# Optimization experiments

Hardware: AMD Instinct MI355X
Metric: run time of the kernel (lower is better)

The kernel has to match this reference:

```python
import jax, jax.numpy as jnp
import numpy as np
from jax import lax

V, D, L = 32000, 1024, 8
HQ, HKV, HD = 16, 4, 64          # head_dim = D // HQ
H = int(2.6875 * D)              # SwiGLU hidden = 2752
B, S = 2, 1024
WINDOW, GEVERY = 256, 4
EPS, BASE = 1e-6, 10000.0
STD = 0.02


def setup_inputs() -> dict:
    key = jax.random.key(0)
    ks = jax.random.split(key, 10)
    return {
        "idx": jax.random.randint(ks[0], (B, S), 0, V, dtype=jnp.int32),
        "emb": jax.random.normal(ks[1], (V, D), jnp.float32) * STD,
        "Wq": jax.random.normal(ks[2], (L, D, HQ * HD), jnp.float32) * STD,
        "Wk": jax.random.normal(ks[3], (L, D, HKV * HD), jnp.float32) * STD,
        "Wv": jax.random.normal(ks[4], (L, D, HKV * HD), jnp.float32) * STD,
        "Wo": jax.random.normal(ks[5], (L, HQ * HD, D), jnp.float32) * (STD / np.sqrt(2 * L)).astype(np.float32),
        "w1": jax.random.normal(ks[6], (L, D, H), jnp.float32) * STD,
        "w3": jax.random.normal(ks[7], (L, D, H), jnp.float32) * STD,
        "w2": jax.random.normal(ks[8], (L, H, D), jnp.float32) * (STD / np.sqrt(2 * L)).astype(np.float32),
        "n1": jnp.ones((L, D), jnp.float32),
        "n2": jnp.ones((L, D), jnp.float32),
        "nf": jnp.ones((D,), jnp.float32),
    }


def _rmsnorm(x, w):
    return x * lax.rsqrt(jnp.mean(x * x, axis=-1, keepdims=True) + EPS) * w


def _rope(x, cos, sin):
    # x: [B,S,h,HD]; pairs (even, odd) rotated by complex multiply with e^{i*theta}
    x2 = x.reshape(*x.shape[:-1], HD // 2, 2)
    x0, x1 = x2[..., 0], x2[..., 1]
    r0 = x0 * cos - x1 * sin
    r1 = x0 * sin + x1 * cos
    return jnp.stack([r0, r1], axis=-1).reshape(x.shape)


def _forward(idx, emb, Wq, Wk, Wv, Wo, w1, w3, w2, n1, n2, nf):
    # RoPE cache (RoPECache._build_cache)
    inv_freq = 1.0 / (BASE ** (jnp.arange(0, HD, 2, dtype=jnp.float32) / HD))
    t = jnp.arange(S, dtype=jnp.float32)
    freqs = t[:, None] * inv_freq[None, :]                      # [S, HD//2]
    cos = jnp.cos(freqs)[None, :, None, :]                      # [1,S,1,HD//2]
    sin = jnp.sin(freqs)[None, :, None, :]

    # masks: global causal and sliding-window causal (additive, 0 / -inf)
    pos = jnp.arange(S)
    causal = pos[None, :] <= pos[:, None]
    local = causal & ((pos[:, None] - pos[None, :]) < WINDOW)
    neg_inf = jnp.float32(-jnp.inf)
    gmask = jnp.where(causal, 0.0, neg_inf).astype(jnp.float32)
    lmask = jnp.where(local, 0.0, neg_inf).astype(jnp.float32)
    use_global = ((jnp.arange(L) + 1) % GEVERY) == 0            # [L] bool

    scale = 1.0 / (HD ** 0.5)
    rep = HQ // HKV

    def block(x, p):
        wq, wk, wv, wo, W1, W3, W2, g1, g2, ug = p
        h = _rmsnorm(x, g1)
        q = (h @ wq).reshape(B, S, HQ, HD)
        k = (h @ wk).reshape(B, S, HKV, HD)
        v = (h @ wv).reshape(B, S, HKV, HD)
        q = _rope(q, cos, sin)
        k = _rope(k, cos, sin)
        k = jnp.repeat(k, rep, axis=2)                          # GQA: expand KV heads
        v = jnp.repeat(v, rep, axis=2)
        mask = jnp.where(ug, gmask, lmask)
        sc = jnp.einsum('bqhd,bkhd->bhqk', q, k) * scale + mask
        attn = jax.nn.softmax(sc, axis=-1)
        o = jnp.einsum('bhqk,bkhd->bqhd', attn, v).reshape(B, S, HQ * HD)
        x = x + o @ wo
        h2 = _rmsnorm(x, g2)
        x = x + (jax.nn.silu(h2 @ W1) * (h2 @ W3)) @ W2
        return x, None

    x = emb[idx]                                                # token embedding
    x, _ = lax.scan(block, x, (Wq, Wk, Wv, Wo, w1, w3, w2, n1, n2, use_global))
    logits = _rmsnorm(x, nf) @ emb.T                            # tied lm_head
    return logits


def reference(idx, emb, Wq, Wk, Wv, Wo, w1, w3, w2, n1, n2, nf):
    return _forward(idx, emb, Wq, Wk, Wv, Wo, w1, w3, w2, n1, n2, nf)
```

## Files before the change

### kernel.cpp

```cpp
#include <hip/hip_runtime.h>

#define V_ 32000
#define D_ 1024
#define L_ 8
#define HQ_ 16
#define HKV_ 4
#define HD_ 64
#define H_ 2752
#define B_ 2
#define S_ 1024
#define BS_ 2048
#define WINDOW_ 256

typedef float f32x4 __attribute__((ext_vector_type(4)));
typedef short s16x8 __attribute__((ext_vector_type(8)));
typedef unsigned short u16;

__device__ __forceinline__ u16 f2b(float f) {
  union { float f; unsigned u; } a; a.f = f;
  return (u16)((a.u + 0x7fffu + ((a.u >> 16) & 1u)) >> 16);
}
__device__ __forceinline__ float b2f(u16 b) {
  union { unsigned u; float f; } a; a.u = ((unsigned)b) << 16; return a.f;
}

__device__ __forceinline__ void gload_lds16(const void* g, void* l) {
  __builtin_amdgcn_global_load_lds(
      (const __attribute__((address_space(1))) void*)(unsigned long long)(uintptr_t)g,
      (__attribute__((address_space(3))) void*)(unsigned int)(uintptr_t)l,
      16, 0, 0);
}

__global__ void k_init(const float* __restrict__ src, u16* __restrict__ dst,
                       float* __restrict__ cosT, float* __restrict__ sinT,
                       const int* __restrict__ idx, float* __restrict__ x) {
  int bid = blockIdx.x;
  if (bid < 32000) {
    long i = (long)bid * 256 + threadIdx.x;
    float4 v = ((const float4*)src)[i];
    ushort4 o; o.x = f2b(v.x); o.y = f2b(v.y); o.z = f2b(v.z); o.w = f2b(v.w);
    ((ushort4*)dst)[i] = o;
  } else if (bid < 32128) {
    int i = (bid - 32000) * 256 + threadIdx.x;
    int s = i >> 5, d = i & 31;
    float inv = __expf(-((float)(2 * d) / (float)HD_) * logf(10000.0f));
    float f = (float)s * inv;
    cosT[i] = cosf(f); sinT[i] = sinf(f);
  } else {
    int t = bid - 32128;
    int token = idx[t];
    const float4* s = (const float4*)(src + (size_t)token * D_);
    float4* d = (float4*)(x + (size_t)t * D_);
    d[threadIdx.x] = s[threadIdx.x];
  }
}

struct TMat { const float* src; u16* dst; int R, C, t0, mul, add; };
struct T7 { TMat m[7]; };

__global__ void k_transpose7(T7 P) {
  __shared__ float tile[32][33];
  int bid = blockIdx.x;
  int mi = 0;
#pragma unroll
  for (int i = 1; i < 7; ++i) if (bid >= P.m[i].t0) mi = i;
  TMat mm = P.m[mi];
  int tl = bid - mm.t0;
  int ct = mm.C >> 5;
  int tr = tl / ct, tc = tl - tr * ct;
  int r0 = tr << 5, c0 = tc << 5;
  int tx = threadIdx.x & 31, ty = threadIdx.x >> 5;
#pragma unroll
  for (int j = 0; j < 4; ++j)
    tile[ty + j * 8][tx] = mm.src[(size_t)(r0 + ty + j * 8) * mm.C + c0 + tx];
  __syncthreads();
#pragma unroll
  for (int j = 0; j < 4; ++j)
    mm.dst[((size_t)(c0 + ty + j * 8) * mm.mul + mm.add) * mm.R + r0 + tx] =
        f2b(tile[tx][ty + j * 8]);
}

__global__ void k_rmsnorm(const float* __restrict__ x, const float* __restrict__ w,
                          u16* __restrict__ out) {
  int row = blockIdx.x, tid = threadIdx.x;
  float4 v = ((const float4*)(x + (size_t)row * D_))[tid];
  float ss = v.x * v.x + v.y * v.y + v.z * v.z + v.w * v.w;
#pragma unroll
  for (int m = 1; m < 64; m <<= 1) ss += __shfl_xor(ss, m, 64);
  __shared__ float red[4];
  if ((tid & 63) == 0) red[tid >> 6] = ss;
  __syncthreads();
  float tot = red[0] + red[1] + red[2] + red[3];
  float rs = rsqrtf(tot * (1.0f / D_) + 1e-6f);
  float4 wv = ((const float4*)w)[tid];
  ushort4 o;
  o.x = f2b(v.x * rs * wv.x); o.y = f2b(v.y * rs * wv.y);
  o.z = f2b(v.z * rs * wv.z); o.w = f2b(v.w * rs * wv.w);
  ((ushort4*)(out + (size_t)row * D_))[tid] = o;
}

__global__ void k_ropev(const float* __restrict__ qkvf, const float* __restrict__ cosT,
                        const float* __restrict__ sinT, u16* __restrict__ qh,
                        u16* __restrict__ kh, u16* __restrict__ vth) {
  __shared__ float tile[32][65];
  int bid = blockIdx.x;
  int tid = threadIdx.x;
  if (bid < BS_) {
    int t = bid;
    int b = t >> 10, s = t & (S_ - 1);
    const float* row = qkvf + (size_t)t * 1536;
    for (int p = tid; p < 512; p += 256) {
      int hh = p >> 5, d = p & 31;
      float x0 = row[hh * 64 + 2 * d], x1 = row[hh * 64 + 2 * d + 1];
      float c = cosT[s * 32 + d], sn = sinT[s * 32 + d];
      size_t o = ((size_t)(b * HQ_ + hh) * S_ + s) * HD_ + 2 * d;
      qh[o] = f2b(x0 * c - x1 * sn);
      qh[o + 1] = f2b(x0 * sn + x1 * c);
    }
    if (tid < 128) {
      int hh = tid >> 5, d = tid & 31;
      float x0 = row[1024 + hh * 64 + 2 * d], x1 = row[1024 + hh * 64 + 2 * d + 1];
      float c = cosT[s * 32 + d], sn = sinT[s * 32 + d];
      size_t o = ((size_t)(b * HKV_ + hh) * S_ + s) * HD_ + 2 * d;
      kh[o] = f2b(x0 * c - x1 * sn);
      kh[o + 1] = f2b(x0 * sn + x1 * c);
    }
  } else {
    int v = bid - BS_;
    const int s0 = (v & 31) << 5, hh = (v >> 5) & 3, b = v >> 7;
    const int tx = tid & 63, ty = tid >> 6;
#pragma unroll
    for (int j = 0; j < 8; ++j) {
      int sl = j * 4 + ty;
      tile[sl][tx] = qkvf[(size_t)((b << 10) + s0 + sl) * 1536 + 1280 + hh * 64 + tx];
    }
    __syncthreads();
    const int sx = tid & 31, dr = tid >> 5;
#pragma unroll
    for (int j = 0; j < 8; ++j) {
      int d = j * 8 + dr;
      vth[((size_t)((b * HKV_ + hh) << 6) + d) * S_ + s0 + sx] = f2b(tile[sx][d]);
    }
  }
}

template <int EPI>
__global__ __launch_bounds__(256) void k_gemm(const u16* __restrict__ A,
                                              const u16* __restrict__ BT,
                                              void* __restrict__ Cp, int kdepth,
                                              int lda, int ldc) {
  __shared__ u16 As[3][4096];
  __shared__ u16 Bs[3][4096];
  const int tid = threadIdx.x;
  const int lane = tid & 63, wid = tid >> 6;
  const int lin = blockIdx.y * 16 + blockIdx.x;
  const int cpx = (gridDim.x * gridDim.y) >> 3;
  const int swz = (lin & 7) * cpx + (lin >> 3);
  const int m0 = (swz & 15) << 7, n0 = (swz >> 4) << 7;
  const int wm = (wid >> 1) << 6, wn = (wid & 1) << 6;
  const int fr = lane & 15, fg = lane >> 4;

  f32x4 acc[4][4] = {};

  const int srow = (wid << 4) + (lane >> 2);
  const int scol = ((lane & 3) - ((lane >> 3) & 3)) & 3;
  const int kz = blockIdx.z * kdepth;
  const u16* ga = A + (size_t)(m0 + srow) * lda + kz + (scol << 3);
  const u16* gb = BT + (size_t)(n0 + srow) * lda + kz + (scol << 3);
  const int cb = wid << 9;

  auto stage = [&](int buf, int k0) {
    u16* la = &As[buf][cb];
    u16* lb = &Bs[buf][cb];
    gload_lds16(ga + k0, la);
    gload_lds16(ga + (size_t)64 * lda + k0, la + 2048);
    gload_lds16(gb + k0, lb);
    gload_lds16(gb + (size_t)64 * lda + k0, lb + 2048);
  };

  const int nk = kdepth >> 5;
  stage(0, 0);
  stage(1, 32);

  const int ab = (wid >> 1) << 2, bb = (wid & 1) << 2;
  const int foff = (fr << 5) + ((((fg + (fr >> 1)) & 3)) << 3);
  int cur = 0;
  for (int t = 0; t < nk; ++t) {
    if (t + 2 < nk) {
      int nb = cur + 2; if (nb >= 3) nb -= 3;
      stage(nb, (t + 2) << 5);
      asm volatile("s_waitcnt vmcnt(8)" ::: "memory");
    } else if (t + 2 == nk) {
      asm volatile("s_waitcnt vmcnt(4)" ::: "memory");
    } else {
      asm volatile("s_waitcnt vmcnt(0)" ::: "memory");
    }
    __builtin_amdgcn_s_barrier();
    s16x8 af[4], bq[4];
#pragma unroll
    for (int i = 0; i < 4; ++i) {
      af[i] = *(const s16x8*)(&As[cur][((ab + i) << 9) + foff]);
      bq[i] = *(const s16x8*)(&Bs[cur][((bb + i) << 9) + foff]);
    }
#pragma unroll
    for (int mi = 0; mi < 4; ++mi)
#pragma unroll
      for (int ni = 0; ni < 4; ++ni)
        acc[mi][ni] = __builtin_amdgcn_mfma_f32_16x16x32_bf16(af[mi], bq[ni], acc[mi][ni], 0, 0, 0);
    __builtin_amdgcn_s_barrier();
    if (++cur == 3) cur = 0;
  }

#pragma unroll
  for (int mi = 0; mi < 4; ++mi) {
#pragma unroll
    for (int ni = 0; ni < 4; ++ni) {
#pragma unroll
      for (int r = 0; r < 4; ++r) {
        int row = m0 + wm + mi * 16 + fg * 4 + r;
        int col = n0 + wn + ni * 16 + fr;
        size_t off = (size_t)row * ldc + col;
        float v = acc[mi][ni][r];
        if (EPI == 0) ((float*)Cp)[off] = v;
        else atomicAdd((float*)Cp + off, v);
      }
    }
  }
}

template <int EPI>
__global__ __launch_bounds__(512, 4) void k_gemm2(const u16* __restrict__ A,
                                                  const u16* __restrict__ BT,
                                                  void* __restrict__ Cp, int K, int ldc) {
  __shared__ u16 As[3][8192];
  __shared__ u16 Bs[3][4096];
  const int tid = threadIdx.x;
  const int lane = tid & 63, wid = tid >> 6;
  const int lin = blockIdx.y * gridDim.x + blockIdx.x;
  const int cpx = (gridDim.x * gridDim.y) >> 3;
  const int swz = (lin & 7) * cpx + (lin >> 3);
  const int m0 = (swz & 7) << 8, n0 = (swz >> 3) << 7;
  const int fr = lane & 15, fg = lane >> 4;

  f32x4 acc[4][4] = {};

  const int srow = lane >> 2;
  const int scol = ((lane & 3) - ((lane >> 3) & 3)) & 3;
  const u16* ga = A + (size_t)(m0 + (wid << 5) + srow) * K + (scol << 3);
  const u16* gb = BT + (size_t)(n0 + (wid << 4) + srow) * K + (scol << 3);
  const int cba = wid << 10;
  const int cbb = wid << 9;

  auto stage = [&](int buf, int k0) {
    gload_lds16(ga + k0, &As[buf][cba]);
    gload_lds16(ga + (size_t)16 * K + k0, &As[buf][cba + 512]);
    gload_lds16(gb + k0, &Bs[buf][cbb]);
  };

  const int nk = K >> 5;
  stage(0, 0);
  stage(1, 32);

  const int am = (wid >> 1) << 2;
  const int bn = (wid & 1) << 2;
  const int foff = (fr << 5) + ((((fg + (fr >> 1)) & 3)) << 3);
  int cur = 0;
  for (int t = 0; t < nk; ++t) {
    if (t + 2 < nk) {
      int nb = cur + 2; if (nb >= 3) nb -= 3;
      stage(nb, (t + 2) << 5);
      asm volatile("s_waitcnt vmcnt(6)" ::: "memory");
    } else if (t + 2 == nk) {
      asm volatile("s_waitcnt vmcnt(3)" ::: "memory");
    } else {
      asm volatile("s_waitcnt vmcnt(0)" ::: "memory");
    }
    __builtin_amdgcn_s_barrier();
    s16x8 af[4], bq[4];
#pragma unroll
    for (int i = 0; i < 4; ++i) {
      af[i] = *(const s16x8*)(&As[cur][((am + i) << 9) + foff]);
      bq[i] = *(const s16x8*)(&Bs[cur][((bn + i) << 9) + foff]);
    }
#pragma unroll
    for (int mi = 0; mi < 4; ++mi)
#pragma unroll
      for (int ni = 0; ni < 4; ++ni)
        acc[mi][ni] = __builtin_amdgcn_mfma_f32_16x16x32_bf16(af[mi], bq[ni], acc[mi][ni], 0, 0, 0);
    __builtin_amdgcn_s_barrier();
    if (++cur == 3) cur = 0;
  }

#pragma unroll
  for (int mi = 0; mi < 4; ++mi) {
#pragma unroll
    for (int ni = 0; ni < 4; ++ni) {
#pragma unroll
      for (int r = 0; r < 4; ++r) {
        int row = m0 + ((wid >> 1) << 6) + mi * 16 + fg * 4 + r;
        int col = n0 + ((wid & 1) << 6) + ni * 16 + fr;
        float v = acc[mi][ni][r];
        if (EPI == 0) {
          ((float*)Cp)[(size_t)row * ldc + col] = v;
        } else {
          float o = __shfl_xor(v, 1, 64);
          if (!(fr & 1)) {
            float s = v / (1.0f + __expf(-v)) * o;
            ((u16*)Cp)[(size_t)row * ldc + (col >> 1)] = f2b(s);
          }
        }
      }
    }
  }
}

__global__ __launch_bounds__(256) void k_attn(const u16* __restrict__ qh,
                                              const u16* __restrict__ kh,
                                              const u16* __restrict__ vth,
                                              u16* __restrict__ attno, int isGlobal) {
  __shared__ u16 pb[4][512];
  const int qblk = blockIdx.x, hq = blockIdx.y, b = blockIdx.z;
  const int lane = threadIdx.x & 63, wid = threadIdx.x >> 6;
  const int fr = lane & 15, fg = lane >> 4;
  const int q0 = (qblk << 6) + (wid << 4);
  const int hk = hq >> 2;
  const u16* Q = qh + ((size_t)(b * HQ_ + hq) * S_) * HD_;
  const u16* Kh = kh + ((size_t)(b * HKV_ + hk) * S_) * HD_;
  const u16* VT = vth + ((size_t)(b * HKV_ + hk) * HD_) * S_;
  u16* pbuf = pb[wid];

  const s16x8 aq0 = *(const s16x8*)(Q + (q0 + fr) * HD_ + fg * 8);
  const s16x8 aq1 = *(const s16x8*)(Q + (q0 + fr) * HD_ + 32 + fg * 8);

  f32x4 o0 = {}, o1 = {}, o2 = {}, o3 = {};
  float m[4], l[4];
#pragma unroll
  for (int r = 0; r < 4; ++r) { m[r] = -1e30f; l[r] = 0.0f; }

  int kt0 = 0;
  if (!isGlobal) { int lo = q0 - (WINDOW_ - 1); if (lo > 0) kt0 = lo & ~31; }
  const int ktend = q0 + 16;

  for (int kt = kt0; kt < ktend; kt += 32) {
    f32x4 sc0 = {}, sc1 = {};
    {
      s16x8 b0 = *(const s16x8*)(Kh + (kt + fr) * HD_ + fg * 8);
      s16x8 b1 = *(const s16x8*)(Kh + (kt + fr) * HD_ + 32 + fg * 8);
      sc0 = __builtin_amdgcn_mfma_f32_16x16x32_bf16(aq0, b0, sc0, 0, 0, 0);
      sc0 = __builtin_amdgcn_mfma_f32_16x16x32_bf16(aq1, b1, sc0, 0, 0, 0);
      s16x8 c0 = *(const s16x8*)(Kh + (kt + 16 + fr) * HD_ + fg * 8);
      s16x8 c1 = *(const s16x8*)(Kh + (kt + 16 + fr) * HD_ + 32 + fg * 8);
      sc1 = __builtin_amdgcn_mfma_f32_16x16x32_bf16(aq0, c0, sc1, 0, 0, 0);
      sc1 = __builtin_amdgcn_mfma_f32_16x16x32_bf16(aq1, c1, sc1, 0, 0, 0);
    }
#pragma unroll
    for (int r = 0; r < 4; ++r) {
      int row = q0 + fg * 4 + r;
      int col0 = kt + fr, col1 = kt + 16 + fr;
      bool v0 = (col0 <= row) && (isGlobal || (row - col0) < WINDOW_);
      bool v1 = (col1 <= row) && (isGlobal || (row - col1) < WINDOW_);
      float s0 = v0 ? sc0[r] * 0.125f : -1e30f;
      float s1 = v1 ? sc1[r] * 0.125f : -1e30f;
      float t = fmaxf(s0, s1);
#pragma unroll
      for (int msk = 1; msk < 16; msk <<= 1) t = fmaxf(t, __shfl_xor(t, msk, 16));
      float mn = fmaxf(m[r], t);
      float fsc = __expf(m[r] - mn);
      m[r] = mn;
      float p0 = v0 ? __expf(s0 - mn) : 0.0f;
      float p1 = v1 ? __expf(s1 - mn) : 0.0f;
      float ps = p0 + p1;
#pragma unroll
      for (int msk = 1; msk < 16; msk <<= 1) ps += __shfl_xor(ps, msk, 16);
      l[r] = l[r] * fsc + ps;
      o0[r] *= fsc; o1[r] *= fsc; o2[r] *= fsc; o3[r] *= fsc;
      pbuf[(fg * 4 + r) * 32 + fr] = f2b(p0);
      pbuf[(fg * 4 + r) * 32 + 16 + fr] = f2b(p1);
    }
    s16x8 ap = *(const s16x8*)(pbuf + fr * 32 + fg * 8);
    {
      s16x8 bv0 = *(const s16x8*)(VT + (size_t)(0 + fr) * S_ + kt + fg * 8);
      o0 = __builtin_amdgcn_mfma_f32_16x16x32_bf16(ap, bv0, o0, 0, 0, 0);
      s16x8 bv1 = *(const s16x8*)(VT + (size_t)(16 + fr) * S_ + kt + fg * 8);
      o1 = __builtin_amdgcn_mfma_f32_16x16x32_bf16(ap, bv1, o1, 0, 0, 0);
      s16x8 bv2 = *(const s16x8*)(VT + (size_t)(32 + fr) * S_ + kt + fg * 8);
      o2 = __builtin_amdgcn_mfma_f32_16x16x32_bf16(ap, bv2, o2, 0, 0, 0);
      s16x8 bv3 = *(const s16x8*)(VT + (size_t)(48 + fr) * S_ + kt + fg * 8);
      o3 = __builtin_amdgcn_mfma_f32_16x16x32_bf16(ap, bv3, o3, 0, 0, 0);
    }
  }

#pragma unroll
  for (int r = 0; r < 4; ++r) {
    int row = q0 + fg * 4 + r;
    float inv = 1.0f / l[r];
    size_t base = ((size_t)b * S_ + row) * (HQ_ * HD_) + hq * HD_;
    attno[base + fr] = f2b(o0[r] * inv);
    attno[base + 16 + fr] = f2b(o1[r] * inv);
    attno[base + 32 + fr] = f2b(o2[r] * inv);
    attno[base + 48 + fr] = f2b(o3[r] * inv);
  }
}

extern "C" void kernel_launch(void* const* d_in, const int* in_sizes, int n_in,
                              void* d_out, int out_size, void* d_ws, size_t ws_size,
                              hipStream_t stream) {
  (void)in_sizes; (void)n_in; (void)out_size; (void)ws_size;
  const int* idx = (const int*)d_in[0];
  const float* emb = (const float*)d_in[1];
  const float* Wq = (const float*)d_in[2];
  const float* Wk = (const float*)d_in[3];
  const float* Wv = (const float*)d_in[4];
  const float* Wo = (const float*)d_in[5];
  const float* w1 = (const float*)d_in[6];
  const float* w3 = (const float*)d_in[7];
  const float* w2 = (const float*)d_in[8];
  const float* n1 = (const float*)d_in[9];
  const float* n2 = (const float*)d_in[10];
  const float* nf = (const float*)d_in[11];
  float* out = (float*)d_out;

  char* p = (char*)d_ws;
  auto carve = [&](size_t bytes) {
    char* q = p;
    p += (bytes + 255) & ~(size_t)255;
    return (void*)q;
  };
  float* x = (float*)carve((size_t)BS_ * D_ * 4);
  u16* h = (u16*)carve((size_t)BS_ * D_ * 2);
  float* qkvf = (float*)carve((size_t)BS_ * 1536 * 4);
  u16* qh = (u16*)carve((size_t)B_ * HQ_ * S_ * HD_ * 2);
  u16* khb = (u16*)carve((size_t)B_ * HKV_ * S_ * HD_ * 2);
  u16* vth = (u16*)carve((size_t)B_ * HKV_ * HD_ * S_ * 2);
  u16* attno = (u16*)carve((size_t)BS_ * D_ * 2);
  u16* g = (u16*)carve((size_t)BS_ * H_ * 2);
  u16* wT = (u16*)carve((size_t)11075584 * 2);
  float* cosT = (float*)carve((size_t)S_ * 32 * 4);
  float* sinT = (float*)carve((size_t)S_ * 32 * 4);
  u16* embb = (u16*)carve((size_t)V_ * D_ * 2);

  k_init<<<32000 + 128 + BS_, 256, 0, stream>>>(emb, embb, cosT, sinT, idx, x);

  for (int l = 0; l < L_; ++l) {
    T7 t7;
    t7.m[0] = { Wq + (size_t)l * D_ * 1024, wT, D_, 1024, 0, 1, 0 };
    t7.m[1] = { Wk + (size_t)l * D_ * 256, wT + 1048576, D_, 256, 1024, 1, 0 };
    t7.m[2] = { Wv + (size_t)l * D_ * 256, wT + 1310720, D_, 256, 1280, 1, 0 };
    t7.m[3] = { Wo + (size_t)l * 1024 * D_, wT + 1572864, 1024, D_, 1536, 1, 0 };
    t7.m[4] = { w1 + (size_t)l * D_ * H_, wT + 2621440, D_, H_, 2560, 2, 0 };
    t7.m[5] = { w3 + (size_t)l * D_ * H_, wT + 2621440, D_, H_, 5312, 2, 1 };
    t7.m[6] = { w2 + (size_t)l * H_ * D_, wT + 8257536, H_, D_, 8064, 1, 0 };
    k_transpose7<<<10816, 256, 0, stream>>>(t7);

    k_rmsnorm<<<BS_, 256, 0, stream>>>(x, n1 + (size_t)l * D_, h);
    k_gemm<0><<<dim3(16, 12), 256, 0, stream>>>(h, wT, qkvf, 1024, 1024, 1536);
    k_ropev<<<BS_ + 256, 256, 0, stream>>>(qkvf, cosT, sinT, qh, khb, vth);
    int ig = ((l + 1) % 4) == 0;
    k_attn<<<dim3(16, HQ_, B_), 256, 0, stream>>>(qh, khb, vth, attno, ig);
    k_gemm<4><<<dim3(16, 8, 2), 256, 0, stream>>>(attno, wT + 1572864, x, 512, 1024, 1024);
    k_rmsnorm<<<BS_, 256, 0, stream>>>(x, n2 + (size_t)l * D_, h);
    k_gemm2<3><<<dim3(8, 43), 512, 0, stream>>>(h, wT + 2621440, g, 1024, 2752);
    k_gemm<4><<<dim3(16, 8, 2), 256, 0, stream>>>(g, wT + 8257536, x, 1376, 2752, 1024);
  }

  k_rmsnorm<<<BS_, 256, 0, stream>>>(x, nf, h);
  k_gemm2<0><<<dim3(8, 250), 512, 0, stream>>>(h, embb, out, 1024, 32000);
}
```

Baseline: 1.494 ms.

## Overlap next-layer weight transpose with down-proj GEMM using double-buffered weights

Removes the standalone per-layer transpose kernel. Layer 0's weight transpose/bf16 conversion is folded into the init kernel, and each later layer's is appended as extra blocks of the previous layer's down-projection GEMM launch. Weights are double-buffered so the next layer's packed weights can be written while the current ones are read. The aim is to fill idle CUs in the small 256-block GEMM with transpose work and cut launch count, at the cost of twice the weight workspace and shared-memory contention between the two block types.

```diff
diff --git a/kernel.cpp b/kernel.cpp
--- a/kernel.cpp
+++ b/kernel.cpp
@@ -11,6 +11,7 @@
 #define S_ 1024
 #define BS_ 2048
 #define WINDOW_ 256
+#define PACK_ 11075584
 
 typedef float f32x4 __attribute__((ext_vector_type(4)));
 typedef short s16x8 __attribute__((ext_vector_type(8)));
@@ -31,9 +32,33 @@
       16, 0, 0);
 }
 
+struct TMat { const float* src; u16* dst; int R, C, t0, mul, add; };
+struct T7 { TMat m[7]; };
+
+__device__ __forceinline__ void transpose_body(const T7& P, int tb,
+                                               float (*tile)[33], int tid) {
+  int mi = 0;
+#pragma unroll
+  for (int i = 1; i < 7; ++i) if (tb >= P.m[i].t0) mi = i;
+  TMat mm = P.m[mi];
+  int tl = tb - mm.t0;
+  int ct = mm.C >> 5;
+  int tr = tl / ct, tc = tl - tr * ct;
+  int r0 = tr << 5, c0 = tc << 5;
+  int tx = tid & 31, ty = tid >> 5;
+#pragma unroll
+  for (int j = 0; j < 4; ++j)
+    tile[ty + j * 8][tx] = mm.src[(size_t)(r0 + ty + j * 8) * mm.C + c0 + tx];
+  __syncthreads();
+#pragma unroll
+  for (int j = 0; j < 4; ++j)
+    mm.dst[((size_t)(c0 + ty + j * 8) * mm.mul + mm.add) * mm.R + r0 + tx] =
+        f2b(tile[tx][ty + j * 8]);
+}
+
 __global__ void k_init(const float* __restrict__ src, u16* __restrict__ dst,
                        float* __restrict__ cosT, float* __restrict__ sinT,
-                       const int* __restrict__ idx, float* __restrict__ x) {
+                       const int* __restrict__ idx, float* __restrict__ x, T7 P0) {
   int bid = blockIdx.x;
   if (bid < 32000) {
     long i = (long)bid * 256 + threadIdx.x;
@@ -46,38 +71,16 @@
     float inv = __expf(-((float)(2 * d) / (float)HD_) * logf(10000.0f));
     float f = (float)s * inv;
     cosT[i] = cosf(f); sinT[i] = sinf(f);
-  } else {
+  } else if (bid < 34176) {
     int t = bid - 32128;
     int token = idx[t];
     const float4* s = (const float4*)(src + (size_t)token * D_);
     float4* d = (float4*)(x + (size_t)t * D_);
     d[threadIdx.x] = s[threadIdx.x];
-  }
-}
-
-struct TMat { const float* src; u16* dst; int R, C, t0, mul, add; };
-struct T7 { TMat m[7]; };
-
-__global__ void k_transpose7(T7 P) {
-  __shared__ float tile[32][33];
-  int bid = blockIdx.x;
-  int mi = 0;
-#pragma unroll
-  for (int i = 1; i < 7; ++i) if (bid >= P.m[i].t0) mi = i;
-  TMat mm = P.m[mi];
-  int tl = bid - mm.t0;
-  int ct = mm.C >> 5;
-  int tr = tl / ct, tc = tl - tr * ct;
-  int r0 = tr << 5, c0 = tc << 5;
-  int tx = threadIdx.x & 31, ty = threadIdx.x >> 5;
-#pragma unroll
-  for (int j = 0; j < 4; ++j)
-    tile[ty + j * 8][tx] = mm.src[(size_t)(r0 + ty + j * 8) * mm.C + c0 + tx];
-  __syncthreads();
-#pragma unroll
-  for (int j = 0; j < 4; ++j)
-    mm.dst[((size_t)(c0 + ty + j * 8) * mm.mul + mm.add) * mm.R + r0 + tx] =
-        f2b(tile[tx][ty + j * 8]);
+  } else {
+    __shared__ float tile[32][33];
+    transpose_body(P0, bid - 34176, tile, threadIdx.x);
+  }
 }
 
 __global__ void k_rmsnorm(const float* __restrict__ x, const float* __restrict__ w,
@@ -145,16 +148,14 @@
 }
 
 template <int EPI>
-__global__ __launch_bounds__(256) void k_gemm(const u16* __restrict__ A,
-                                              const u16* __restrict__ BT,
-                                              void* __restrict__ Cp, int kdepth,
-                                              int lda, int ldc) {
-  __shared__ u16 As[3][4096];
-  __shared__ u16 Bs[3][4096];
+__device__ __forceinline__ void gemm128_body(const u16* __restrict__ A,
+                                             const u16* __restrict__ BT,
+                                             void* __restrict__ Cp, int kdepth,
+                                             int lda, int ldc, int bx, int by, int bz,
+                                             int cpx, u16 (*As)[4096], u16 (*Bs)[4096]) {
   const int tid = threadIdx.x;
   const int lane = tid & 63, wid = tid >> 6;
-  const int lin = blockIdx.y * 16 + blockIdx.x;
-  const int cpx = (gridDim.x * gridDim.y) >> 3;
+  const int lin = by * 16 + bx;
   const int swz = (lin & 7) * cpx + (lin >> 3);
   const int m0 = (swz & 15) << 7, n0 = (swz >> 4) << 7;
   const int wm = (wid >> 1) << 6, wn = (wid & 1) << 6;
@@ -164,7 +165,7 @@
 
   const int srow = (wid << 4) + (lane >> 2);
   const int scol = ((lane & 3) - ((lane >> 3) & 3)) & 3;
-  const int kz = blockIdx.z * kdepth;
+  const int kz = bz * kdepth;
   const u16* ga = A + (size_t)(m0 + srow) * lda + kz + (scol << 3);
   const u16* gb = BT + (size_t)(n0 + srow) * lda + kz + (scol << 3);
   const int cb = wid << 9;
@@ -226,6 +227,33 @@
       }
     }
   }
+}
+
+template <int EPI>
+__global__ __launch_bounds__(256) void k_gemm(const u16* __restrict__ A,
+                                              const u16* __restrict__ BT,
+                                              void* __restrict__ Cp, int kdepth,
+                                              int lda, int ldc) {
+  __shared__ u16 As[3][4096];
+  __shared__ u16 Bs[3][4096];
+  gemm128_body<EPI>(A, BT, Cp, kdepth, lda, ldc, blockIdx.x, blockIdx.y, blockIdx.z,
+                    (gridDim.x * gridDim.y) >> 3, As, Bs);
+}
+
+__global__ __launch_bounds__(256) void k_gemmtr(const u16* __restrict__ A,
+                                                const u16* __restrict__ BT,
+                                                void* __restrict__ Cp, int kdepth,
+                                                int lda, int ldc, T7 P) {
+  __shared__ u16 As[3][4096];
+  __shared__ u16 Bs[3][4096];
+  int bid = blockIdx.x;
+  if (bid >= 256) {
+    __shared__ float tile[32][33];
+    transpose_body(P, bid - 256, tile, threadIdx.x);
+    return;
+  }
+  gemm128_body<4>(A, BT, Cp, kdepth, lda, ldc, bid & 15, (bid & 127) >> 4, bid >> 7,
+                  16, As, Bs);
 }
 
 template <int EPI>
@@ -434,33 +462,41 @@
   u16* vth = (u16*)carve((size_t)B_ * HKV_ * HD_ * S_ * 2);
   u16* attno = (u16*)carve((size_t)BS_ * D_ * 2);
   u16* g = (u16*)carve((size_t)BS_ * H_ * 2);
-  u16* wT = (u16*)carve((size_t)11075584 * 2);
+  u16* wT = (u16*)carve((size_t)PACK_ * 2 * 2);
   float* cosT = (float*)carve((size_t)S_ * 32 * 4);
   float* sinT = (float*)carve((size_t)S_ * 32 * 4);
   u16* embb = (u16*)carve((size_t)V_ * D_ * 2);
 
-  k_init<<<32000 + 128 + BS_, 256, 0, stream>>>(emb, embb, cosT, sinT, idx, x);
+  auto makeT7 = [&](int l, u16* base) {
+    T7 t7;
+    t7.m[0] = { Wq + (size_t)l * D_ * 1024, base, D_, 1024, 0, 1, 0 };
+    t7.m[1] = { Wk + (size_t)l * D_ * 256, base + 1048576, D_, 256, 1024, 1, 0 };
+    t7.m[2] = { Wv + (size_t)l * D_ * 256, base + 1310720, D_, 256, 1280, 1, 0 };
+    t7.m[3] = { Wo + (size_t)l * 1024 * D_, base + 1572864, 1024, D_, 1536, 1, 0 };
+    t7.m[4] = { w1 + (size_t)l * D_ * H_, base + 2621440, D_, H_, 2560, 2, 0 };
+    t7.m[5] = { w3 + (size_t)l * D_ * H_, base + 2621440, D_, H_, 5312, 2, 1 };
+    t7.m[6] = { w2 + (size_t)l * H_ * D_, base + 8257536, H_, D_, 8064, 1, 0 };
+    return t7;
+  };
+
+  k_init<<<34176 + 10816, 256, 0, stream>>>(emb, embb, cosT, sinT, idx, x,
+                                            makeT7(0, wT));
 
   for (int l = 0; l < L_; ++l) {
-    T7 t7;
-    t7.m[0] = { Wq + (size_t)l * D_ * 1024, wT, D_, 1024, 0, 1, 0 };
-    t7.m[1] = { Wk + (size_t)l * D_ * 256, wT + 1048576, D_, 256, 1024, 1, 0 };
-    t7.m[2] = { Wv + (size_t)l * D_ * 256, wT + 1310720, D_, 256, 1280, 1, 0 };
-    t7.m[3] = { Wo + (size_t)l * 1024 * D_, wT + 1572864, 1024, D_, 1536, 1, 0 };
-    t7.m[4] = { w1 + (size_t)l * D_ * H_, wT + 2621440, D_, H_, 2560, 2, 0 };
-    t7.m[5] = { w3 + (size_t)l * D_ * H_, wT + 2621440, D_, H_, 5312, 2, 1 };
-    t7.m[6] = { w2 + (size_t)l * H_ * D_, wT + 8257536, H_, D_, 8064, 1, 0 };
-    k_transpose7<<<10816, 256, 0, stream>>>(t7);
+    u16* wTl = wT + (size_t)(l & 1) * PACK_;
 
     k_rmsnorm<<<BS_, 256, 0, stream>>>(x, n1 + (size_t)l * D_, h);
-    k_gemm<0><<<dim3(16, 12), 256, 0, stream>>>(h, wT, qkvf, 1024, 1024, 1536);
+    k_gemm<0><<<dim3(16, 12), 256, 0, stream>>>(h, wTl, qkvf, 1024, 1024, 1536);
     k_ropev<<<BS_ + 256, 256, 0, stream>>>(qkvf, cosT, sinT, qh, khb, vth);
     int ig = ((l + 1) % 4) == 0;
     k_attn<<<dim3(16, HQ_, B_), 256, 0, stream>>>(qh, khb, vth, attno, ig);
-    k_gemm<4><<<dim3(16, 8, 2), 256, 0, stream>>>(attno, wT + 1572864, x, 512, 1024, 1024);
+    k_gemm<4><<<dim3(16, 8, 2), 256, 0, stream>>>(attno, wTl + 1572864, x, 512, 1024, 1024);
     k_rmsnorm<<<BS_, 256, 0, stream>>>(x, n2 + (size_t)l * D_, h);
-    k_gemm2<3><<<dim3(8, 43), 512, 0, stream>>>(h, wT + 2621440, g, 1024, 2752);
-    k_gemm<4><<<dim3(16, 8, 2), 256, 0, stream>>>(g, wT + 8257536, x, 1376, 2752, 1024);
+    k_gemm2<3><<<dim3(8, 43), 512, 0, stream>>>(h, wTl + 2621440, g, 1024, 2752);
+    const bool doTr = (l + 1) < L_;
+    u16* wTn = wT + (size_t)((l + 1) & 1) * PACK_;
+    k_gemmtr<<<doTr ? (256 + 10816) : 256, 256, 0, stream>>>(
+        g, wTl + 8257536, x, 1376, 2752, 1024, makeT7(doTr ? l + 1 : 0, wTn));
   }
 
   k_rmsnorm<<<BS_, 256, 0, stream>>>(x, nf, h);
```

New measurement: 1.492 ms. About the same (-0.1%).
